# Performance work log

Measured on AMD Instinct MI355X. Metric: run time of the kernel, lower is better.

## Reference

```python
import jax, jax.numpy as jnp
import numpy as np

N = 8192
D = 256

def setup_inputs() -> dict:
    key = jax.random.key(0)
    k1, k2, k3 = jax.random.split(key, 3)
    x = jax.random.normal(k1, (N, D), dtype=jnp.float32)
    adj_t = jax.random.uniform(k2, (N, N), dtype=jnp.float32)
    adj_t2 = jax.random.uniform(k3, (N, N), dtype=jnp.float32)
    return {"x": x, "adj_t": adj_t, "adj_t2": adj_t2}

def reference(x, adj_t, adj_t2):
    # H2GCN neighborhood aggregation: 1-hop and 2-hop adjacency matmuls, concat on feature dim.
    x1 = adj_t @ x    # [N, D]
    x2 = adj_t2 @ x   # [N, D]
    return jnp.concatenate([x1, x2], axis=1)  # [N, 2D]
```

## Files before the change

kernel.cpp:

```cpp
#include <hip/hip_runtime.h>
#include <stdint.h>
#include <stddef.h>

#define N_TOT  8192
#define D_FEAT 256
#define BM 32
#define BK 64
#define LDK 72
#define K_ITERS (N_TOT / BK)

typedef float f32x4_t __attribute__((ext_vector_type(4)));
typedef short s16x8_t __attribute__((ext_vector_type(8)));

__device__ __forceinline__ unsigned short f2bf(float f) {
    union { float f; unsigned int u; } a;
    a.f = f;
    unsigned int r = a.u + 0x7FFFu + ((a.u >> 16) & 1u);
    return (unsigned short)(r >> 16);
}

__global__ __launch_bounds__(256) void xpose_kernel(
    const float* __restrict__ x, unsigned short* __restrict__ xT)
{
    __shared__ unsigned short T[64 * 72];
    const int t  = threadIdx.x;
    const int k0 = blockIdx.x * 64;
    const int n0 = blockIdx.y * 64;

    #pragma unroll
    for (int i = 0; i < 4; ++i) {
        const int kr = (t >> 4) + 16 * i;
        const int c4 = (t & 15) * 4;
        float4 v = *(const float4*)(x + (size_t)(k0 + kr) * D_FEAT + n0 + c4);
        T[(c4 + 0) * 72 + kr] = f2bf(v.x);
        T[(c4 + 1) * 72 + kr] = f2bf(v.y);
        T[(c4 + 2) * 72 + kr] = f2bf(v.z);
        T[(c4 + 3) * 72 + kr] = f2bf(v.w);
    }
    __syncthreads();
    #pragma unroll
    for (int i = 0; i < 2; ++i) {
        const int n  = (t >> 3) + 32 * i;
        const int c8 = (t & 7) * 8;
        uint4 w = *(const uint4*)&T[n * 72 + c8];
        *(uint4*)(xT + (size_t)(n0 + n) * N_TOT + k0 + c8) = w;
    }
}

__global__ __launch_bounds__(512, 4) void h2gcn_kernel(
    const float* __restrict__ adj0,
    const float* __restrict__ adj1,
    const unsigned short* __restrict__ xT,
    float* __restrict__ out)
{
    const int g  = blockIdx.y;
    const float* __restrict__ adj = g ? adj1 : adj0;
    const int m0   = blockIdx.x * BM;
    const int t    = threadIdx.x;
    const int lane = t & 63;
    const int w    = t >> 6;
    const int fl   = lane & 15;
    const int fq   = lane >> 4;

    __shared__ __align__(16) unsigned short Asm[BM * LDK];

    const int a_row = t >> 4;
    const int a_c4  = (t & 15) * 4;

    const float* aBase = adj + (size_t)m0 * N_TOT + (size_t)a_row * N_TOT + a_c4;

    const unsigned short* bBase0 = xT + (size_t)(32 * w + fl) * N_TOT + 8 * fq;
    const unsigned short* bBase1 = bBase0 + (size_t)16 * N_TOT;

    float4 a_reg = *(const float4*)aBase;

    s16x8_t b[2][2][2];
    #pragma unroll
    for (int ks = 0; ks < 2; ++ks) {
        b[0][0][ks] = *(const s16x8_t*)(bBase0 + 32 * ks);
        b[0][1][ks] = *(const s16x8_t*)(bBase1 + 32 * ks);
    }

    f32x4_t acc[2][2];
    #pragma unroll
    for (int mt = 0; mt < 2; ++mt)
        #pragma unroll
        for (int nt = 0; nt < 2; ++nt) {
            f32x4_t z = {0.0f, 0.0f, 0.0f, 0.0f};
            acc[mt][nt] = z;
        }

    #pragma unroll 2
    for (int it = 0; it < K_ITERS; ++it) {
        const int cur = it & 1;
        const int nxt = cur ^ 1;

        __syncthreads();
        {
            ushort4 v;
            v.x = f2bf(a_reg.x); v.y = f2bf(a_reg.y);
            v.z = f2bf(a_reg.z); v.w = f2bf(a_reg.w);
            *(ushort4*)&Asm[a_row * LDK + a_c4] = v;
        }
        __syncthreads();

        if (it + 1 < K_ITERS) {
            const size_t k0 = (size_t)(it + 1) * BK;
            a_reg = *(const float4*)(aBase + k0);
            #pragma unroll
            for (int ks = 0; ks < 2; ++ks) {
                b[nxt][0][ks] = *(const s16x8_t*)(bBase0 + k0 + 32 * ks);
                b[nxt][1][ks] = *(const s16x8_t*)(bBase1 + k0 + 32 * ks);
            }
        }

        s16x8_t af[2][2];
        #pragma unroll
        for (int mt = 0; mt < 2; ++mt)
            #pragma unroll
            for (int ks = 0; ks < 2; ++ks)
                af[mt][ks] = *(const s16x8_t*)&Asm[(16 * mt + fl) * LDK + 32 * ks + 8 * fq];

        #pragma unroll
        for (int ks = 0; ks < 2; ++ks)
            #pragma unroll
            for (int mt = 0; mt < 2; ++mt)
                #pragma unroll
                for (int nt = 0; nt < 2; ++nt)
                    acc[mt][nt] = __builtin_amdgcn_mfma_f32_16x16x32_bf16(
                        af[mt][ks], b[cur][nt][ks], acc[mt][nt], 0, 0, 0);
    }

    #pragma unroll
    for (int mt = 0; mt < 2; ++mt)
        #pragma unroll
        for (int nt = 0; nt < 2; ++nt)
            #pragma unroll
            for (int r = 0; r < 4; ++r) {
                const int row = m0 + 16 * mt + 4 * fq + r;
                const int col = g * D_FEAT + 32 * w + 16 * nt + fl;
                out[(size_t)row * (2 * D_FEAT) + col] = acc[mt][nt][r];
            }
}

extern "C" void kernel_launch(void* const* d_in, const int* in_sizes, int n_in,
                              void* d_out, int out_size, void* d_ws, size_t ws_size,
                              hipStream_t stream) {
    const float* x      = (const float*)d_in[0];
    const float* adj_t  = (const float*)d_in[1];
    const float* adj_t2 = (const float*)d_in[2];
    float* out = (float*)d_out;
    unsigned short* xT = (unsigned short*)d_ws;
    (void)in_sizes; (void)n_in; (void)out_size; (void)ws_size;

    hipLaunchKernelGGL(xpose_kernel, dim3(N_TOT / 64, D_FEAT / 64), dim3(256), 0, stream, x, xT);
    hipLaunchKernelGGL(h2gcn_kernel, dim3(N_TOT / BM, 2), dim3(512), 0, stream,
                       adj_t, adj_t2, xT, out);
}
```

Baseline: 681.3 us.

## Double-buffer A tile in LDS with deeper register prefetch and single barrier

Converts the single LDS A tile into a double buffer, so each iteration writes the next tile while reading the current one. This replaces the two __syncthreads per iteration with one explicit waitcnt plus s_barrier. The adjacency loads are prefetched three iterations ahead using nontemporal loads, to hide HBM latency and avoid cache pollution from the streamed 256 MB adjacency matrices. The risks are more register and LDS use per block, which may lower occupancy under launch_bounds(512,4), and subtle ordering hazards from the hand-placed barrier.

New measurement: 658.7 us. 3.3% less time.

```diff
diff --git a/kernel.cpp b/kernel.cpp
--- a/kernel.cpp
+++ b/kernel.cpp
@@ -17,6 +17,10 @@
     a.f = f;
     unsigned int r = a.u + 0x7FFFu + ((a.u >> 16) & 1u);
     return (unsigned short)(r >> 16);
+}
+
+__device__ __forceinline__ f32x4_t ldg_nt(const float* p) {
+    return __builtin_nontemporal_load((const f32x4_t*)p);
 }
 
 __global__ __launch_bounds__(256) void xpose_kernel(
@@ -62,26 +66,19 @@
     const int fl   = lane & 15;
     const int fq   = lane >> 4;
 
-    __shared__ __align__(16) unsigned short Asm[BM * LDK];
+    __shared__ __align__(16) unsigned short Asm[2][BM * LDK];
 
     const int a_row = t >> 4;
     const int a_c4  = (t & 15) * 4;
-
-    const float* aBase = adj + (size_t)m0 * N_TOT + (size_t)a_row * N_TOT + a_c4;
+    const float* aBase = adj + (size_t)(m0 + a_row) * N_TOT + a_c4;
 
     const unsigned short* bBase0 = xT + (size_t)(32 * w + fl) * N_TOT + 8 * fq;
     const unsigned short* bBase1 = bBase0 + (size_t)16 * N_TOT;
 
-    float4 a_reg = *(const float4*)aBase;
+    f32x4_t aR[2];
+    s16x8_t bR[2][2][2];
+    f32x4_t acc[2][2];
 
-    s16x8_t b[2][2][2];
-    #pragma unroll
-    for (int ks = 0; ks < 2; ++ks) {
-        b[0][0][ks] = *(const s16x8_t*)(bBase0 + 32 * ks);
-        b[0][1][ks] = *(const s16x8_t*)(bBase1 + 32 * ks);
-    }
-
-    f32x4_t acc[2][2];
     #pragma unroll
     for (int mt = 0; mt < 2; ++mt)
         #pragma unroll
@@ -90,28 +87,32 @@
             acc[mt][nt] = z;
         }
 
+    f32x4_t a0 = ldg_nt(aBase);
+    aR[1]      = ldg_nt(aBase + BK);
+    aR[0]      = ldg_nt(aBase + 2 * BK);
+    #pragma unroll
+    for (int ks = 0; ks < 2; ++ks) {
+        bR[0][0][ks] = *(const s16x8_t*)(bBase0 + 32 * ks);
+        bR[0][1][ks] = *(const s16x8_t*)(bBase1 + 32 * ks);
+    }
+    {
+        ushort4 v;
+        v.x = f2bf(a0.x); v.y = f2bf(a0.y);
+        v.z = f2bf(a0.z); v.w = f2bf(a0.w);
+        *(ushort4*)&Asm[0][a_row * LDK + a_c4] = v;
+    }
+    __syncthreads();
+
     #pragma unroll 2
     for (int it = 0; it < K_ITERS; ++it) {
         const int cur = it & 1;
         const int nxt = cur ^ 1;
 
-        __syncthreads();
         {
             ushort4 v;
-            v.x = f2bf(a_reg.x); v.y = f2bf(a_reg.y);
-            v.z = f2bf(a_reg.z); v.w = f2bf(a_reg.w);
-            *(ushort4*)&Asm[a_row * LDK + a_c4] = v;
-        }
-        __syncthreads();
-
-        if (it + 1 < K_ITERS) {
-            const size_t k0 = (size_t)(it + 1) * BK;
-            a_reg = *(const float4*)(aBase + k0);
-            #pragma unroll
-            for (int ks = 0; ks < 2; ++ks) {
-                b[nxt][0][ks] = *(const s16x8_t*)(bBase0 + k0 + 32 * ks);
-                b[nxt][1][ks] = *(const s16x8_t*)(bBase1 + k0 + 32 * ks);
-            }
+            v.x = f2bf(aR[nxt].x); v.y = f2bf(aR[nxt].y);
+            v.z = f2bf(aR[nxt].z); v.w = f2bf(aR[nxt].w);
+            *(ushort4*)&Asm[nxt][a_row * LDK + a_c4] = v;
         }
 
         s16x8_t af[2][2];
@@ -119,7 +120,22 @@
         for (int mt = 0; mt < 2; ++mt)
             #pragma unroll
             for (int ks = 0; ks < 2; ++ks)
-                af[mt][ks] = *(const s16x8_t*)&Asm[(16 * mt + fl) * LDK + 32 * ks + 8 * fq];
+                af[mt][ks] = *(const s16x8_t*)&Asm[cur][(16 * mt + fl) * LDK + 32 * ks + 8 * fq];
+
+        const int ta = (it + 3 < K_ITERS) ? (it + 3) : (K_ITERS - 1);
+        const int tb = (it + 1 < K_ITERS) ? (it + 1) : (K_ITERS - 1);
+        const size_t ka = (size_t)ta * BK;
+        const size_t kb = (size_t)tb * BK;
+        aR[nxt] = ldg_nt(aBase + ka);
+        #pragma unroll
+        for (int ks = 0; ks < 2; ++ks) {
+            bR[nxt][0][ks] = *(const s16x8_t*)(bBase0 + kb + 32 * ks);
+            bR[nxt][1][ks] = *(const s16x8_t*)(bBase1 + kb + 32 * ks);
+        }
+
+        asm volatile("s_waitcnt lgkmcnt(0)" ::: "memory");
+        __builtin_amdgcn_sched_barrier(0);
+        __builtin_amdgcn_s_barrier();
 
         #pragma unroll
         for (int ks = 0; ks < 2; ++ks)
@@ -128,7 +144,7 @@
                 #pragma unroll
                 for (int nt = 0; nt < 2; ++nt)
                     acc[mt][nt] = __builtin_amdgcn_mfma_f32_16x16x32_bf16(
-                        af[mt][ks], b[cur][nt][ks], acc[mt][nt], 0, 0, 0);
+                        af[mt][ks], bR[cur][nt][ks], acc[mt][nt], 0, 0, 0);
     }
 
     #pragma unroll
```
